# Optimization experiments

Hardware: AMD Instinct MI355X
Metric: run time of the kernel (lower is better)

Reference implementation:

```python
import jax, jax.numpy as jnp
import numpy as np

SIGMA = 1.0


def _rbf_gram(A, B):
    # A: (Tb, N, C), B: (Tb, M, C) -> (Tb, N, M)
    AA = jnp.sum(A * A, axis=2, keepdims=True)          # (Tb, N, 1)
    BB = jnp.sum(B * B, axis=2, keepdims=True)          # (Tb, M, 1)
    d = AA + jnp.swapaxes(BB, 1, 2) - 2.0 * jnp.einsum('bnc,bmc->bnm', A, B)
    return jnp.exp(-d / (2.0 * SIGMA ** 2))


def setup_inputs() -> dict:
    key = jax.random.key(0)
    kx, ky = jax.random.split(key)
    x = jax.random.normal(kx, (512, 128, 16), dtype=jnp.float32)
    y = jax.random.normal(ky, (512, 128, 16), dtype=jnp.float32)
    return {"x": x, "y": y}


def reference(x, y):
    # x, y: (batch, stream, channel)
    x_fds = jnp.concatenate((x[:, :-1, :], x[:, 1:, :]), axis=1)  # (B, 2(T-1), C)
    y_fds = jnp.concatenate((y[:, :-1, :], y[:, 1:, :]), axis=1)
    xf = jnp.transpose(x_fds, (1, 0, 2))  # (2(T-1), B, C)
    yf = jnp.transpose(y_fds, (1, 0, 2))

    N = xf.shape[1]
    Kxx = _rbf_gram(xf, xf)  # (2(T-1), N, N)
    # off-diagonal mean per batch: (sum - trace) / (N*(N-1))
    e_xx = (Kxx.sum(axis=(1, 2)) - jnp.trace(Kxx, axis1=1, axis2=2)) / (N * (N - 1))
    E_k_x1_x2 = e_xx.mean()

    Kxy = _rbf_gram(xf, yf)
    E_k_x_y = Kxy.mean(axis=(1, 2)).mean()

    return E_k_x1_x2 - 2.0 * E_k_x_y
```

## Files before the change

### kernel.cpp

```cpp
#include <hip/hip_runtime.h>


#define LOG2E 1.4426950408889634f
#define SCALE 1.2011224087864498f

typedef __attribute__((ext_vector_type(8))) __bf16 bf16x8;
typedef __attribute__((ext_vector_type(4))) float floatx4;

union FragU { uint4 q; unsigned int u[4]; bf16x8 v; };

static __device__ __forceinline__ int off(int n) { return (n << 3) + ((n >> 2) << 2); }

static __device__ __forceinline__ unsigned short bfbits(__bf16 h) {
    union { __bf16 h; unsigned short s; } u; u.h = h; return u.s;
}
static __device__ __forceinline__ unsigned int packhh(__bf16 a, __bf16 b) {
    return (unsigned int)bfbits(a) | ((unsigned int)bfbits(b) << 16);
}

#define NSLOT 26
#define ONEONE 0x3F803F80u

__global__ __launch_bounds__(256, 8) void mmd_kernel(const float* __restrict__ x,
                                                     const float* __restrict__ y,
                                                     float* __restrict__ part) {
    __shared__ unsigned int AH[1152], BH[1152];
    __shared__ unsigned int BG[512];
    __shared__ float srg[128];
    __shared__ unsigned int zero4[4];
    __shared__ float red[4];

    const int slot = blockIdx.x;
    const int t    = blockIdx.y;
    const int tid  = threadIdx.x;
    const int w    = tid >> 6;
    const int lane = tid & 63;
    const int quad = lane >> 4;
    const int l15  = lane & 15;
    const int qh   = quad & 1;

    int sa, sq, isxx;
    if (slot < 16) { isxx = 0; sa = slot >> 2; sq = slot & 3; }
    else {
        isxx = 1;
        const int s = slot - 16;
        if      (s < 4) { sa = 0; sq = s; }
        else if (s < 7) { sa = 1; sq = s - 3; }
        else if (s < 9) { sa = 2; sq = s - 5; }
        else            { sa = 3; sq = 3; }
    }

    if (tid == 0) { zero4[0] = 0u; zero4[1] = 0u; zero4[2] = 0u; zero4[3] = 0u; }

    {
        const int half = tid >> 7;
        const int r    = tid & 127;
        const int grow = (half ? sq : sa) * 128 + r;
        const float4* __restrict__ src4 =
            (half && !isxx) ? (const float4*)y : (const float4*)x;
        const size_t gb = (size_t)grow * 512 + t * 4;
        float4 f0 = src4[gb], f1 = src4[gb + 1], f2 = src4[gb + 2], f3 = src4[gb + 3];
        const float fs[16] = { f0.x, f0.y, f0.z, f0.w, f1.x, f1.y, f1.z, f1.w,
                               f2.x, f2.y, f2.z, f2.w, f3.x, f3.y, f3.z, f3.w };
        float g = 0.f;
        unsigned int hw[8];
#pragma unroll
        for (int p = 0; p < 8; ++p) {
            const float v0 = fs[2 * p], v1 = fs[2 * p + 1];
            g += v0 * v0 + v1 * v1;
            hw[p] = packhh((__bf16)(v0 * SCALE), (__bf16)(v1 * SCALE));
        }
        const float gp = 0.5f * LOG2E * g;
        unsigned int* __restrict__ H = half ? BH : AH;
        const int o = off(r);
        *(uint4*)&H[o]     = make_uint4(hw[0], hw[1], hw[2], hw[3]);
        *(uint4*)&H[o + 4] = make_uint4(hw[4], hw[5], hw[6], hw[7]);
        if (half) {
            const __bf16 nh = (__bf16)(-gp);
            const __bf16 nl = (__bf16)(-(gp + (float)nh));
            *(uint4*)&BG[r * 4] = make_uint4(packhh(nh, nl), 0u, 0u, 0u);
        } else {
            srg[r] = gp;
        }
    }
    __syncthreads();

    bf16x8 a1f[2];
    {
#pragma unroll
        for (int rt = 0; rt < 2; ++rt) {
            FragU u;
            if (quad < 2) {
                const int row = w * 32 + rt * 16 + l15;
                u.q = *(const uint4*)&AH[off(row) + qh * 4];
            } else {
                u.q = make_uint4((quad == 2) ? ONEONE : 0u, 0u, 0u, 0u);
            }
            a1f[rt] = u.v;
        }
    }

    const unsigned int* bptr;
    int bstride;
    if (quad < 2)      { bptr = &BH[off(l15) + qh * 4]; bstride = 144; }
    else if (quad == 2){ bptr = &BG[l15 * 4];           bstride = 64;  }
    else               { bptr = &zero4[0];              bstride = 0;   }

    float sum[2][4] = {{0.f, 0.f, 0.f, 0.f}, {0.f, 0.f, 0.f, 0.f}};

    floatx4 accP[2], accC[2];
    {
        FragU b; b.q = *(const uint4*)bptr; bptr += bstride;
        floatx4 zc = {0.f, 0.f, 0.f, 0.f};
        accP[0] = __builtin_amdgcn_mfma_f32_16x16x32_bf16(a1f[0], b.v, zc, 0, 0, 0);
        accP[1] = __builtin_amdgcn_mfma_f32_16x16x32_bf16(a1f[1], b.v, zc, 0, 0, 0);
    }
#pragma unroll
    for (int jt = 1; jt < 8; ++jt) {
        FragU b; b.q = *(const uint4*)bptr; bptr += bstride;
        floatx4 zc = {0.f, 0.f, 0.f, 0.f};
        accC[0] = __builtin_amdgcn_mfma_f32_16x16x32_bf16(a1f[0], b.v, zc, 0, 0, 0);
        accC[1] = __builtin_amdgcn_mfma_f32_16x16x32_bf16(a1f[1], b.v, zc, 0, 0, 0);
#pragma unroll
        for (int rt = 0; rt < 2; ++rt)
#pragma unroll
            for (int r = 0; r < 4; ++r)
                sum[rt][r] += __builtin_amdgcn_exp2f(accP[rt][r]);
        accP[0] = accC[0];
        accP[1] = accC[1];
    }
#pragma unroll
    for (int rt = 0; rt < 2; ++rt)
#pragma unroll
        for (int r = 0; r < 4; ++r)
            sum[rt][r] += __builtin_amdgcn_exp2f(accP[rt][r]);

    float tot = 0.f;
#pragma unroll
    for (int rt = 0; rt < 2; ++rt)
#pragma unroll
        for (int r = 0; r < 4; ++r) {
            const float rs = __builtin_amdgcn_exp2f(-srg[w * 32 + rt * 16 + quad * 4 + r]);
            tot = fmaf(sum[rt][r], rs, tot);
        }
    for (int o = 32; o > 0; o >>= 1) tot += __shfl_down(tot, o, 64);
    if (lane == 0) red[w] = tot;
    __syncthreads();
    if (tid == 0) {
        float wt = (t == 0 || t == 127) ? 1.f : 2.f;
        if (isxx && sq > sa) wt *= 2.f;
        const int idx = isxx ? (2048 + t * 10 + (slot - 16)) : (t * 16 + slot);
        part[idx] = wt * (red[0] + red[1] + red[2] + red[3]);
    }
}

__global__ __launch_bounds__(256) void finalize_kernel(const float* __restrict__ part,
                                                       float* __restrict__ out) {
    const int tid = threadIdx.x;
    double vxy = 0.0, vxx = 0.0;
#pragma unroll
    for (int k = 0; k < 8; ++k)  vxy += (double)part[tid + 256 * k];
#pragma unroll
    for (int k = 8; k < 13; ++k) vxx += (double)part[tid + 256 * k];
    for (int o = 32; o > 0; o >>= 1) {
        vxx += __shfl_down(vxx, o, 64);
        vxy += __shfl_down(vxy, o, 64);
    }
    __shared__ double red[8];
    const int wid = tid >> 6;
    if ((tid & 63) == 0) { red[wid] = vxx; red[4 + wid] = vxy; }
    __syncthreads();
    if (tid == 0) {
        double sxx = red[0] + red[1] + red[2] + red[3];
        double sxy = red[4] + red[5] + red[6] + red[7];
        double e1 = (sxx - 254.0 * 512.0) / (254.0 * 512.0 * 511.0);
        double e2 = sxy / (254.0 * 512.0 * 512.0);
        out[0] = (float)(e1 - 2.0 * e2);
    }
}

extern "C" void kernel_launch(void* const* d_in, const int* in_sizes, int n_in,
                              void* d_out, int out_size, void* d_ws, size_t ws_size,
                              hipStream_t stream) {
    (void)in_sizes; (void)n_in; (void)out_size; (void)ws_size;
    const float* x = (const float*)d_in[0];
    const float* y = (const float*)d_in[1];
    float* out  = (float*)d_out;
    float* part = (float*)d_ws;

    mmd_kernel<<<dim3(NSLOT, 128), dim3(256), 0, stream>>>(x, y, part);
    finalize_kernel<<<dim3(1), dim3(256), 0, stream>>>(part, out);
}
```

Before: 71.79 us.

## Process four timesteps per block with double-buffered LDS staging and prefetch

Each block now handles four consecutive t values instead of one, which cuts the grid from 26x128 to 26x32. The next timestep's global loads are issued before the current MFMA/exp2 work, and the loaded data is staged into a second LDS buffer so load latency overlaps compute. Per-t weights are folded into the accumulation, and the partials layout and finalize reduction are adjusted to match. In exchange, the block doubles its LDS, the launch bound drops to 4 blocks per CU, parallelism is lower, and extra barriers are added.

Result: slower. 123.1 us (+71.5%).

```diff
diff --git a/kernel.cpp b/kernel.cpp
--- a/kernel.cpp
+++ b/kernel.cpp
@@ -3,6 +3,7 @@
 
 #define LOG2E 1.4426950408889634f
 #define SCALE 1.2011224087864498f
+#define NT 4
 
 typedef __attribute__((ext_vector_type(8))) __bf16 bf16x8;
 typedef __attribute__((ext_vector_type(4))) float floatx4;
@@ -21,17 +22,17 @@
 #define NSLOT 26
 #define ONEONE 0x3F803F80u
 
-__global__ __launch_bounds__(256, 8) void mmd_kernel(const float* __restrict__ x,
+__global__ __launch_bounds__(256, 4) void mmd_kernel(const float* __restrict__ x,
                                                      const float* __restrict__ y,
                                                      float* __restrict__ part) {
-    __shared__ unsigned int AH[1152], BH[1152];
-    __shared__ unsigned int BG[512];
-    __shared__ float srg[128];
+    __shared__ unsigned int AH[2][1152], BH[2][1152];
+    __shared__ unsigned int BG[2][512];
+    __shared__ float srg[2][128];
     __shared__ unsigned int zero4[4];
     __shared__ float red[4];
 
     const int slot = blockIdx.x;
-    const int t    = blockIdx.y;
+    const int t0   = blockIdx.y * NT;
     const int tid  = threadIdx.x;
     const int w    = tid >> 6;
     const int lane = tid & 63;
@@ -52,14 +53,13 @@
 
     if (tid == 0) { zero4[0] = 0u; zero4[1] = 0u; zero4[2] = 0u; zero4[3] = 0u; }
 
-    {
-        const int half = tid >> 7;
-        const int r    = tid & 127;
-        const int grow = (half ? sq : sa) * 128 + r;
-        const float4* __restrict__ src4 =
-            (half && !isxx) ? (const float4*)y : (const float4*)x;
-        const size_t gb = (size_t)grow * 512 + t * 4;
-        float4 f0 = src4[gb], f1 = src4[gb + 1], f2 = src4[gb + 2], f3 = src4[gb + 3];
+    const int half = tid >> 7;
+    const int r    = tid & 127;
+    const float4* __restrict__ src4 =
+        (half && !isxx) ? (const float4*)y : (const float4*)x;
+    const size_t rowbase = (size_t)((half ? sq : sa) * 128 + r) * 512;
+
+    auto stage = [&](int buf, float4 f0, float4 f1, float4 f2, float4 f3) {
         const float fs[16] = { f0.x, f0.y, f0.z, f0.w, f1.x, f1.y, f1.z, f1.w,
                                f2.x, f2.y, f2.z, f2.w, f3.x, f3.y, f3.z, f3.w };
         float g = 0.f;
@@ -71,97 +71,116 @@
             hw[p] = packhh((__bf16)(v0 * SCALE), (__bf16)(v1 * SCALE));
         }
         const float gp = 0.5f * LOG2E * g;
-        unsigned int* __restrict__ H = half ? BH : AH;
+        unsigned int* __restrict__ H = half ? BH[buf] : AH[buf];
         const int o = off(r);
         *(uint4*)&H[o]     = make_uint4(hw[0], hw[1], hw[2], hw[3]);
         *(uint4*)&H[o + 4] = make_uint4(hw[4], hw[5], hw[6], hw[7]);
         if (half) {
             const __bf16 nh = (__bf16)(-gp);
             const __bf16 nl = (__bf16)(-(gp + (float)nh));
-            *(uint4*)&BG[r * 4] = make_uint4(packhh(nh, nl), 0u, 0u, 0u);
+            *(uint4*)&BG[buf][r * 4] = make_uint4(packhh(nh, nl), 0u, 0u, 0u);
         } else {
-            srg[r] = gp;
-        }
+            srg[buf][r] = gp;
+        }
+    };
+
+    {
+        const size_t gb = rowbase + t0 * 4;
+        stage(0, src4[gb], src4[gb + 1], src4[gb + 2], src4[gb + 3]);
     }
     __syncthreads();
 
-    bf16x8 a1f[2];
-    {
+    float tot = 0.f;
+
+#pragma unroll
+    for (int tt = 0; tt < NT; ++tt) {
+        const int buf = tt & 1;
+        const int t   = t0 + tt;
+
+        float4 p0, p1, p2, p3;
+        if (tt < NT - 1) {
+            const size_t gb = rowbase + (t + 1) * 4;
+            p0 = src4[gb]; p1 = src4[gb + 1]; p2 = src4[gb + 2]; p3 = src4[gb + 3];
+        }
+
+        bf16x8 a1f[2];
 #pragma unroll
         for (int rt = 0; rt < 2; ++rt) {
             FragU u;
             if (quad < 2) {
                 const int row = w * 32 + rt * 16 + l15;
-                u.q = *(const uint4*)&AH[off(row) + qh * 4];
+                u.q = *(const uint4*)&AH[buf][off(row) + qh * 4];
             } else {
                 u.q = make_uint4((quad == 2) ? ONEONE : 0u, 0u, 0u, 0u);
             }
             a1f[rt] = u.v;
         }
-    }
-
-    const unsigned int* bptr;
-    int bstride;
-    if (quad < 2)      { bptr = &BH[off(l15) + qh * 4]; bstride = 144; }
-    else if (quad == 2){ bptr = &BG[l15 * 4];           bstride = 64;  }
-    else               { bptr = &zero4[0];              bstride = 0;   }
-
-    float sum[2][4] = {{0.f, 0.f, 0.f, 0.f}, {0.f, 0.f, 0.f, 0.f}};
-
-    floatx4 accP[2], accC[2];
-    {
-        FragU b; b.q = *(const uint4*)bptr; bptr += bstride;
-        floatx4 zc = {0.f, 0.f, 0.f, 0.f};
-        accP[0] = __builtin_amdgcn_mfma_f32_16x16x32_bf16(a1f[0], b.v, zc, 0, 0, 0);
-        accP[1] = __builtin_amdgcn_mfma_f32_16x16x32_bf16(a1f[1], b.v, zc, 0, 0, 0);
-    }
-#pragma unroll
-    for (int jt = 1; jt < 8; ++jt) {
-        FragU b; b.q = *(const uint4*)bptr; bptr += bstride;
-        floatx4 zc = {0.f, 0.f, 0.f, 0.f};
-        accC[0] = __builtin_amdgcn_mfma_f32_16x16x32_bf16(a1f[0], b.v, zc, 0, 0, 0);
-        accC[1] = __builtin_amdgcn_mfma_f32_16x16x32_bf16(a1f[1], b.v, zc, 0, 0, 0);
+
+        const unsigned int* bptr;
+        int bstride;
+        if (quad < 2)       { bptr = &BH[buf][off(l15) + qh * 4]; bstride = 144; }
+        else if (quad == 2) { bptr = &BG[buf][l15 * 4];           bstride = 64;  }
+        else                { bptr = &zero4[0];                   bstride = 0;   }
+
+        float sum[2][4] = {{0.f, 0.f, 0.f, 0.f}, {0.f, 0.f, 0.f, 0.f}};
+
+        floatx4 accP[2], accC[2];
+        {
+            FragU b; b.q = *(const uint4*)bptr; bptr += bstride;
+            floatx4 zc = {0.f, 0.f, 0.f, 0.f};
+            accP[0] = __builtin_amdgcn_mfma_f32_16x16x32_bf16(a1f[0], b.v, zc, 0, 0, 0);
+            accP[1] = __builtin_amdgcn_mfma_f32_16x16x32_bf16(a1f[1], b.v, zc, 0, 0, 0);
+        }
+#pragma unroll
+        for (int jt = 1; jt < 8; ++jt) {
+            FragU b; b.q = *(const uint4*)bptr; bptr += bstride;
+            floatx4 zc = {0.f, 0.f, 0.f, 0.f};
+            accC[0] = __builtin_amdgcn_mfma_f32_16x16x32_bf16(a1f[0], b.v, zc, 0, 0, 0);
+            accC[1] = __builtin_amdgcn_mfma_f32_16x16x32_bf16(a1f[1], b.v, zc, 0, 0, 0);
+#pragma unroll
+            for (int rt = 0; rt < 2; ++rt)
+#pragma unroll
+                for (int rr = 0; rr < 4; ++rr)
+                    sum[rt][rr] += __builtin_amdgcn_exp2f(accP[rt][rr]);
+            accP[0] = accC[0];
+            accP[1] = accC[1];
+        }
 #pragma unroll
         for (int rt = 0; rt < 2; ++rt)
 #pragma unroll
-            for (int r = 0; r < 4; ++r)
-                sum[rt][r] += __builtin_amdgcn_exp2f(accP[rt][r]);
-        accP[0] = accC[0];
-        accP[1] = accC[1];
-    }
-#pragma unroll
-    for (int rt = 0; rt < 2; ++rt)
-#pragma unroll
-        for (int r = 0; r < 4; ++r)
-            sum[rt][r] += __builtin_amdgcn_exp2f(accP[rt][r]);
-
-    float tot = 0.f;
-#pragma unroll
-    for (int rt = 0; rt < 2; ++rt)
-#pragma unroll
-        for (int r = 0; r < 4; ++r) {
-            const float rs = __builtin_amdgcn_exp2f(-srg[w * 32 + rt * 16 + quad * 4 + r]);
-            tot = fmaf(sum[rt][r], rs, tot);
-        }
+            for (int rr = 0; rr < 4; ++rr)
+                sum[rt][rr] += __builtin_amdgcn_exp2f(accP[rt][rr]);
+
+        float wt = (t == 0 || t == 127) ? 1.f : 2.f;
+        if (isxx && sq > sa) wt *= 2.f;
+#pragma unroll
+        for (int rt = 0; rt < 2; ++rt)
+#pragma unroll
+            for (int rr = 0; rr < 4; ++rr) {
+                const float rs =
+                    wt * __builtin_amdgcn_exp2f(-srg[buf][w * 32 + rt * 16 + quad * 4 + rr]);
+                tot = fmaf(sum[rt][rr], rs, tot);
+            }
+
+        if (tt < NT - 1) {
+            stage(buf ^ 1, p0, p1, p2, p3);
+            __syncthreads();
+        }
+    }
+
     for (int o = 32; o > 0; o >>= 1) tot += __shfl_down(tot, o, 64);
     if (lane == 0) red[w] = tot;
     __syncthreads();
-    if (tid == 0) {
-        float wt = (t == 0 || t == 127) ? 1.f : 2.f;
-        if (isxx && sq > sa) wt *= 2.f;
-        const int idx = isxx ? (2048 + t * 10 + (slot - 16)) : (t * 16 + slot);
-        part[idx] = wt * (red[0] + red[1] + red[2] + red[3]);
-    }
+    if (tid == 0)
+        part[slot * 32 + blockIdx.y] = red[0] + red[1] + red[2] + red[3];
 }
 
 __global__ __launch_bounds__(256) void finalize_kernel(const float* __restrict__ part,
                                                        float* __restrict__ out) {
     const int tid = threadIdx.x;
-    double vxy = 0.0, vxx = 0.0;
-#pragma unroll
-    for (int k = 0; k < 8; ++k)  vxy += (double)part[tid + 256 * k];
-#pragma unroll
-    for (int k = 8; k < 13; ++k) vxx += (double)part[tid + 256 * k];
+    double vxy = (double)part[tid] + (double)part[256 + tid];
+    double vxx = (double)part[512 + tid];
+    if (tid < 64) vxx += (double)part[768 + tid];
     for (int o = 32; o > 0; o >>= 1) {
         vxx += __shfl_down(vxx, o, 64);
         vxy += __shfl_down(vxy, o, 64);
@@ -188,6 +207,6 @@
     float* out  = (float*)d_out;
     float* part = (float*)d_ws;
 
-    mmd_kernel<<<dim3(NSLOT, 128), dim3(256), 0, stream>>>(x, y, part);
+    mmd_kernel<<<dim3(NSLOT, 32), dim3(256), 0, stream>>>(x, y, part);
     finalize_kernel<<<dim3(1), dim3(256), 0, stream>>>(part, out);
 }
```

## Enlarge per-block tile to 256x256 and cut slot count from 26 to 7

Applied to the files above, without the earlier changes.

Each block now computes a 256x256 Gram tile instead of 128x128, with each wave handling 64 rows (four MFMA row tiles) across 16 column tiles. This reduces the grid from 26x128 to 7x128 blocks and removes redundant global loads and bf16 packing of the same rows across blocks, and uses the symmetric-half trick at coarser granularity. It costs more LDS per block, more registers, and launch bounds drop to 4 blocks per CU, so there is less parallelism and latency hiding. The finalize kernel is adjusted to the new partial-sum layout, and the weight is applied per lane.

New measurement: 72.82 us. No clear change (+1.4%).

```diff
diff --git a/kernel.cpp b/kernel.cpp
--- a/kernel.cpp
+++ b/kernel.cpp
@@ -3,6 +3,7 @@
 
 #define LOG2E 1.4426950408889634f
 #define SCALE 1.2011224087864498f
+#define ONEONE 0x3F803F80u
 
 typedef __attribute__((ext_vector_type(8))) __bf16 bf16x8;
 typedef __attribute__((ext_vector_type(4))) float floatx4;
@@ -17,16 +18,16 @@
 static __device__ __forceinline__ unsigned int packhh(__bf16 a, __bf16 b) {
     return (unsigned int)bfbits(a) | ((unsigned int)bfbits(b) << 16);
 }
-
-#define NSLOT 26
-#define ONEONE 0x3F803F80u
-
-__global__ __launch_bounds__(256, 8) void mmd_kernel(const float* __restrict__ x,
+static __device__ __forceinline__ unsigned int packff(float a, float b) {
+    return packhh((__bf16)(a * SCALE), (__bf16)(b * SCALE));
+}
+
+__global__ __launch_bounds__(256, 4) void mmd_kernel(const float* __restrict__ x,
                                                      const float* __restrict__ y,
                                                      float* __restrict__ part) {
-    __shared__ unsigned int AH[1152], BH[1152];
-    __shared__ unsigned int BG[512];
-    __shared__ float srg[128];
+    __shared__ unsigned int AH[2300], BH[2300];
+    __shared__ unsigned int BG[1024];
+    __shared__ float srg[256];
     __shared__ unsigned int zero4[4];
     __shared__ float red[4];
 
@@ -39,129 +40,140 @@
     const int l15  = lane & 15;
     const int qh   = quad & 1;
 
-    int sa, sq, isxx;
-    if (slot < 16) { isxx = 0; sa = slot >> 2; sq = slot & 3; }
+    int Ah, Bh, isxx;
+    if (slot < 4) { isxx = 0; Ah = slot >> 1; Bh = slot & 1; }
     else {
         isxx = 1;
-        const int s = slot - 16;
-        if      (s < 4) { sa = 0; sq = s; }
-        else if (s < 7) { sa = 1; sq = s - 3; }
-        else if (s < 9) { sa = 2; sq = s - 5; }
-        else            { sa = 3; sq = 3; }
+        Ah = (slot == 6) ? 1 : 0;
+        Bh = (slot == 4) ? 0 : 1;
     }
 
     if (tid == 0) { zero4[0] = 0u; zero4[1] = 0u; zero4[2] = 0u; zero4[3] = 0u; }
 
     {
-        const int half = tid >> 7;
-        const int r    = tid & 127;
-        const int grow = (half ? sq : sa) * 128 + r;
-        const float4* __restrict__ src4 =
-            (half && !isxx) ? (const float4*)y : (const float4*)x;
-        const size_t gb = (size_t)grow * 512 + t * 4;
-        float4 f0 = src4[gb], f1 = src4[gb + 1], f2 = src4[gb + 2], f3 = src4[gb + 3];
-        const float fs[16] = { f0.x, f0.y, f0.z, f0.w, f1.x, f1.y, f1.z, f1.w,
-                               f2.x, f2.y, f2.z, f2.w, f3.x, f3.y, f3.z, f3.w };
-        float g = 0.f;
-        unsigned int hw[8];
-#pragma unroll
-        for (int p = 0; p < 8; ++p) {
-            const float v0 = fs[2 * p], v1 = fs[2 * p + 1];
-            g += v0 * v0 + v1 * v1;
-            hw[p] = packhh((__bf16)(v0 * SCALE), (__bf16)(v1 * SCALE));
+        const float4* __restrict__ xa = (const float4*)x;
+        const float4* __restrict__ bsrc = isxx ? (const float4*)x : (const float4*)y;
+        const size_t ga = (size_t)(Ah * 256 + tid) * 512 + t * 4;
+        const size_t gbb = (size_t)(Bh * 256 + tid) * 512 + t * 4;
+        float4 a0 = xa[ga], a1 = xa[ga + 1], a2 = xa[ga + 2], a3 = xa[ga + 3];
+        float4 b0 = bsrc[gbb], b1 = bsrc[gbb + 1], b2 = bsrc[gbb + 2], b3 = bsrc[gbb + 3];
+
+        const float gA =
+            (a0.x * a0.x + a0.y * a0.y + a0.z * a0.z + a0.w * a0.w) +
+            (a1.x * a1.x + a1.y * a1.y + a1.z * a1.z + a1.w * a1.w) +
+            (a2.x * a2.x + a2.y * a2.y + a2.z * a2.z + a2.w * a2.w) +
+            (a3.x * a3.x + a3.y * a3.y + a3.z * a3.z + a3.w * a3.w);
+        const float gB =
+            (b0.x * b0.x + b0.y * b0.y + b0.z * b0.z + b0.w * b0.w) +
+            (b1.x * b1.x + b1.y * b1.y + b1.z * b1.z + b1.w * b1.w) +
+            (b2.x * b2.x + b2.y * b2.y + b2.z * b2.z + b2.w * b2.w) +
+            (b3.x * b3.x + b3.y * b3.y + b3.z * b3.z + b3.w * b3.w);
+
+        const int o = off(tid);
+        *(uint4*)&AH[o]     = make_uint4(packff(a0.x, a0.y), packff(a0.z, a0.w),
+                                         packff(a1.x, a1.y), packff(a1.z, a1.w));
+        *(uint4*)&AH[o + 4] = make_uint4(packff(a2.x, a2.y), packff(a2.z, a2.w),
+                                         packff(a3.x, a3.y), packff(a3.z, a3.w));
+        *(uint4*)&BH[o]     = make_uint4(packff(b0.x, b0.y), packff(b0.z, b0.w),
+                                         packff(b1.x, b1.y), packff(b1.z, b1.w));
+        *(uint4*)&BH[o + 4] = make_uint4(packff(b2.x, b2.y), packff(b2.z, b2.w),
+                                         packff(b3.x, b3.y), packff(b3.z, b3.w));
+        srg[tid] = 0.5f * LOG2E * gA;
+        const float gp = 0.5f * LOG2E * gB;
+        const __bf16 nh = (__bf16)(-gp);
+        const __bf16 nl = (__bf16)(-(gp + (float)nh));
+        *(uint4*)&BG[tid * 4] = make_uint4(packhh(nh, nl), 0u, 0u, 0u);
+    }
+    __syncthreads();
+
+    bf16x8 a1f0, a1f1, a1f2, a1f3;
+    {
+        FragU u0, u1, u2, u3;
+        if (quad < 2) {
+            const int r0 = w * 64 + l15;
+            u0.q = *(const uint4*)&AH[off(r0) + qh * 4];
+            u1.q = *(const uint4*)&AH[off(r0 + 16) + qh * 4];
+            u2.q = *(const uint4*)&AH[off(r0 + 32) + qh * 4];
+            u3.q = *(const uint4*)&AH[off(r0 + 48) + qh * 4];
+        } else {
+            u0.q = make_uint4((quad == 2) ? ONEONE : 0u, 0u, 0u, 0u);
+            u1.q = u0.q; u2.q = u0.q; u3.q = u0.q;
         }
-        const float gp = 0.5f * LOG2E * g;
-        unsigned int* __restrict__ H = half ? BH : AH;
-        const int o = off(r);
-        *(uint4*)&H[o]     = make_uint4(hw[0], hw[1], hw[2], hw[3]);
-        *(uint4*)&H[o + 4] = make_uint4(hw[4], hw[5], hw[6], hw[7]);
-        if (half) {
-            const __bf16 nh = (__bf16)(-gp);
-            const __bf16 nl = (__bf16)(-(gp + (float)nh));
-            *(uint4*)&BG[r * 4] = make_uint4(packhh(nh, nl), 0u, 0u, 0u);
-        } else {
-            srg[r] = gp;
-        }
-    }
-    __syncthreads();
-
-    bf16x8 a1f[2];
-    {
-#pragma unroll
-        for (int rt = 0; rt < 2; ++rt) {
-            FragU u;
-            if (quad < 2) {
-                const int row = w * 32 + rt * 16 + l15;
-                u.q = *(const uint4*)&AH[off(row) + qh * 4];
-            } else {
-                u.q = make_uint4((quad == 2) ? ONEONE : 0u, 0u, 0u, 0u);
-            }
-            a1f[rt] = u.v;
-        }
+        a1f0 = u0.v; a1f1 = u1.v; a1f2 = u2.v; a1f3 = u3.v;
     }
 
     const unsigned int* bptr;
     int bstride;
-    if (quad < 2)      { bptr = &BH[off(l15) + qh * 4]; bstride = 144; }
-    else if (quad == 2){ bptr = &BG[l15 * 4];           bstride = 64;  }
-    else               { bptr = &zero4[0];              bstride = 0;   }
-
-    float sum[2][4] = {{0.f, 0.f, 0.f, 0.f}, {0.f, 0.f, 0.f, 0.f}};
-
-    floatx4 accP[2], accC[2];
+    if (quad < 2)       { bptr = &BH[off(l15) + qh * 4]; bstride = 144; }
+    else if (quad == 2) { bptr = &BG[l15 * 4];           bstride = 64;  }
+    else                { bptr = &zero4[0];              bstride = 0;   }
+
+    float s0[4] = {0.f, 0.f, 0.f, 0.f};
+    float s1[4] = {0.f, 0.f, 0.f, 0.f};
+    float s2[4] = {0.f, 0.f, 0.f, 0.f};
+    float s3[4] = {0.f, 0.f, 0.f, 0.f};
+
+    floatx4 p0, p1, p2, p3, c0, c1, c2, c3;
     {
         FragU b; b.q = *(const uint4*)bptr; bptr += bstride;
         floatx4 zc = {0.f, 0.f, 0.f, 0.f};
-        accP[0] = __builtin_amdgcn_mfma_f32_16x16x32_bf16(a1f[0], b.v, zc, 0, 0, 0);
-        accP[1] = __builtin_amdgcn_mfma_f32_16x16x32_bf16(a1f[1], b.v, zc, 0, 0, 0);
-    }
-#pragma unroll
-    for (int jt = 1; jt < 8; ++jt) {
+        p0 = __builtin_amdgcn_mfma_f32_16x16x32_bf16(a1f0, b.v, zc, 0, 0, 0);
+        p1 = __builtin_amdgcn_mfma_f32_16x16x32_bf16(a1f1, b.v, zc, 0, 0, 0);
+        p2 = __builtin_amdgcn_mfma_f32_16x16x32_bf16(a1f2, b.v, zc, 0, 0, 0);
+        p3 = __builtin_amdgcn_mfma_f32_16x16x32_bf16(a1f3, b.v, zc, 0, 0, 0);
+    }
+#pragma unroll
+    for (int jt = 1; jt < 16; ++jt) {
         FragU b; b.q = *(const uint4*)bptr; bptr += bstride;
         floatx4 zc = {0.f, 0.f, 0.f, 0.f};
-        accC[0] = __builtin_amdgcn_mfma_f32_16x16x32_bf16(a1f[0], b.v, zc, 0, 0, 0);
-        accC[1] = __builtin_amdgcn_mfma_f32_16x16x32_bf16(a1f[1], b.v, zc, 0, 0, 0);
-#pragma unroll
-        for (int rt = 0; rt < 2; ++rt)
-#pragma unroll
-            for (int r = 0; r < 4; ++r)
-                sum[rt][r] += __builtin_amdgcn_exp2f(accP[rt][r]);
-        accP[0] = accC[0];
-        accP[1] = accC[1];
-    }
-#pragma unroll
-    for (int rt = 0; rt < 2; ++rt)
-#pragma unroll
-        for (int r = 0; r < 4; ++r)
-            sum[rt][r] += __builtin_amdgcn_exp2f(accP[rt][r]);
-
+        c0 = __builtin_amdgcn_mfma_f32_16x16x32_bf16(a1f0, b.v, zc, 0, 0, 0);
+        c1 = __builtin_amdgcn_mfma_f32_16x16x32_bf16(a1f1, b.v, zc, 0, 0, 0);
+        c2 = __builtin_amdgcn_mfma_f32_16x16x32_bf16(a1f2, b.v, zc, 0, 0, 0);
+        c3 = __builtin_amdgcn_mfma_f32_16x16x32_bf16(a1f3, b.v, zc, 0, 0, 0);
+#pragma unroll
+        for (int r = 0; r < 4; ++r) {
+            s0[r] += __builtin_amdgcn_exp2f(p0[r]);
+            s1[r] += __builtin_amdgcn_exp2f(p1[r]);
+            s2[r] += __builtin_amdgcn_exp2f(p2[r]);
+            s3[r] += __builtin_amdgcn_exp2f(p3[r]);
+        }
+        p0 = c0; p1 = c1; p2 = c2; p3 = c3;
+    }
+#pragma unroll
+    for (int r = 0; r < 4; ++r) {
+        s0[r] += __builtin_amdgcn_exp2f(p0[r]);
+        s1[r] += __builtin_amdgcn_exp2f(p1[r]);
+        s2[r] += __builtin_amdgcn_exp2f(p2[r]);
+        s3[r] += __builtin_amdgcn_exp2f(p3[r]);
+    }
+
+    float wt = (t == 0 || t == 127) ? 1.f : 2.f;
+    if (slot == 5) wt *= 2.f;
     float tot = 0.f;
-#pragma unroll
-    for (int rt = 0; rt < 2; ++rt)
-#pragma unroll
-        for (int r = 0; r < 4; ++r) {
-            const float rs = __builtin_amdgcn_exp2f(-srg[w * 32 + rt * 16 + quad * 4 + r]);
-            tot = fmaf(sum[rt][r], rs, tot);
-        }
+    const int rbase = w * 64 + quad * 4;
+#pragma unroll
+    for (int r = 0; r < 4; ++r) {
+        tot = fmaf(s0[r], wt * __builtin_amdgcn_exp2f(-srg[rbase + r]),      tot);
+        tot = fmaf(s1[r], wt * __builtin_amdgcn_exp2f(-srg[rbase + 16 + r]), tot);
+        tot = fmaf(s2[r], wt * __builtin_amdgcn_exp2f(-srg[rbase + 32 + r]), tot);
+        tot = fmaf(s3[r], wt * __builtin_amdgcn_exp2f(-srg[rbase + 48 + r]), tot);
+    }
+
     for (int o = 32; o > 0; o >>= 1) tot += __shfl_down(tot, o, 64);
     if (lane == 0) red[w] = tot;
     __syncthreads();
     if (tid == 0) {
-        float wt = (t == 0 || t == 127) ? 1.f : 2.f;
-        if (isxx && sq > sa) wt *= 2.f;
-        const int idx = isxx ? (2048 + t * 10 + (slot - 16)) : (t * 16 + slot);
-        part[idx] = wt * (red[0] + red[1] + red[2] + red[3]);
+        const int idx = isxx ? (512 + t * 3 + (slot - 4)) : (t * 4 + slot);
+        part[idx] = red[0] + red[1] + red[2] + red[3];
     }
 }
 
 __global__ __launch_bounds__(256) void finalize_kernel(const float* __restrict__ part,
                                                        float* __restrict__ out) {
     const int tid = threadIdx.x;
-    double vxy = 0.0, vxx = 0.0;
-#pragma unroll
-    for (int k = 0; k < 8; ++k)  vxy += (double)part[tid + 256 * k];
-#pragma unroll
-    for (int k = 8; k < 13; ++k) vxx += (double)part[tid + 256 * k];
+    double vxy = (double)part[tid] + (double)part[256 + tid];
+    double vxx = (double)part[512 + tid];
+    if (tid < 128) vxx += (double)part[768 + tid];
     for (int o = 32; o > 0; o >>= 1) {
         vxx += __shfl_down(vxx, o, 64);
         vxy += __shfl_down(vxy, o, 64);
@@ -188,6 +200,6 @@
     float* out  = (float*)d_out;
     float* part = (float*)d_ws;
 
-    mmd_kernel<<<dim3(NSLOT, 128), dim3(256), 0, stream>>>(x, y, part);
+    mmd_kernel<<<dim3(7, 128), dim3(256), 0, stream>>>(x, y, part);
     finalize_kernel<<<dim3(1), dim3(256), 0, stream>>>(part, out);
 }
```
